# Performance work log

Measured on AMD Instinct MI355X. Metric: run time of the kernel, lower is better.

## Reference

```python
import jax, jax.numpy as jnp
import numpy as np

N = 50000
E = 800000
D_IN, D_HID, D_OUT = 256, 512, 256
LN_EPS = 1e-5


def setup_inputs() -> dict:
    key = jax.random.key(0)
    ks = jax.random.split(key, 8)
    return {
        "v": jax.random.normal(ks[0], (N, D_IN), dtype=jnp.float32),
        "edge_weight": jax.random.uniform(ks[1], (E,), dtype=jnp.float32),
        "epsilon": jnp.zeros((1, 1), dtype=jnp.float32),
        "w1": jax.random.normal(ks[2], (D_HID, D_IN), dtype=jnp.float32) * (1.0 / np.sqrt(D_IN)),
        "b1": jnp.zeros((D_HID,), dtype=jnp.float32),
        "g1": jnp.ones((D_HID,), dtype=jnp.float32),
        "beta1": jnp.zeros((D_HID,), dtype=jnp.float32),
        "w2": jax.random.normal(ks[3], (D_OUT, D_HID), dtype=jnp.float32) * (1.0 / np.sqrt(D_HID)),
        "b2": jnp.zeros((D_OUT,), dtype=jnp.float32),
        "g2": jnp.ones((D_OUT,), dtype=jnp.float32),
        "beta2": jnp.zeros((D_OUT,), dtype=jnp.float32),
        "src": jax.random.randint(ks[4], (E,), 0, N, dtype=jnp.int32),
        "dst": jax.random.randint(ks[5], (E,), 0, N, dtype=jnp.int32),
    }


def _layer_norm(x, g, b):
    mu = jnp.mean(x, axis=-1, keepdims=True)
    var = jnp.mean(jnp.square(x - mu), axis=-1, keepdims=True)
    return (x - mu) * jax.lax.rsqrt(var + LN_EPS) * g + b


def reference(v, edge_weight, epsilon, w1, b1, g1, beta1, w2, b2, g2, beta2, src, dst):
    # sparse adjacency aggregation: agg[dst] += w * v[src]   (torch.sparse.mm(a, v))
    msgs = v[src] * edge_weight[:, None]            # [E, D_IN]
    agg = jax.ops.segment_sum(msgs, dst, num_segments=v.shape[0])  # [N, D_IN]
    h = agg + epsilon * v                            # epsilon residual
    # MLP: Linear -> LayerNorm -> ReLU  (x2)
    h = jax.nn.relu(_layer_norm(h @ w1.T + b1, g1, beta1))
    h = jax.nn.relu(_layer_norm(h @ w2.T + b2, g2, beta2))
    return h
```

## Files before the change

### kernel.cpp

```cpp
#include <hip/hip_runtime.h>

#define D_IN 256
#define D_HID 512
#define D_OUT 256
#define LN_EPS 1e-5f
#define SCAN_B 512

typedef __attribute__((ext_vector_type(8))) short bf16x8;
typedef __attribute__((ext_vector_type(4))) float f32x4;

__device__ __forceinline__ ushort f2bf(float x) {
    union { float f; unsigned u; } c; c.f = x;
    unsigned r = c.u + 0x7FFFu + ((c.u >> 16) & 1u);
    return (ushort)(r >> 16);
}
__device__ __forceinline__ float bf2f(unsigned b) {
    union { unsigned u; float f; } c; c.u = b << 16;
    return c.f;
}

__global__ void prep_kernel(const float* __restrict__ v, const float* __restrict__ w1,
                            const float* __restrict__ w2, ushort* __restrict__ vb,
                            ushort* __restrict__ w1b, ushort* __restrict__ w2b,
                            int* __restrict__ cnt, int n4v, int nzero,
                            int bv, int bw) {
    int b = blockIdx.x, t = threadIdx.x;
    if (b < bv) {
        int i = b * 256 + t;
        if (i < n4v) {
            float4 x = ((const float4*)v)[i];
            ((ushort4*)vb)[i] = make_ushort4(f2bf(x.x), f2bf(x.y), f2bf(x.z), f2bf(x.w));
        }
    } else if (b < bv + bw) {
        int j = (b - bv) * 256 + t;
        if (j < 32768) {
            float4 x = ((const float4*)w1)[j];
            ((ushort4*)w1b)[j] = make_ushort4(f2bf(x.x), f2bf(x.y), f2bf(x.z), f2bf(x.w));
        } else {
            int k = j - 32768;
            float4 x = ((const float4*)w2)[k];
            ((ushort4*)w2b)[k] = make_ushort4(f2bf(x.x), f2bf(x.y), f2bf(x.z), f2bf(x.w));
        }
    } else {
        int i = (b - bv - bw) * 256 + t;
        if (i < nzero) cnt[i] = 0;
    }
}

__global__ void hist_kernel(const int* __restrict__ dst, int* __restrict__ cnt, int E) {
    int e = blockIdx.x * 256 + threadIdx.x;
    if (e < E) atomicAdd(&cnt[dst[e]], 1);
}

__global__ __launch_bounds__(SCAN_B) void scan1_kernel(const int* __restrict__ cnt,
                                                       int* __restrict__ offs,
                                                       int* __restrict__ bsum, int n) {
    __shared__ int s[SCAN_B];
    int i = blockIdx.x * SCAN_B + threadIdx.x;
    int x = (i < n) ? cnt[i] : 0;
    s[threadIdx.x] = x;
    __syncthreads();
    for (int o = 1; o < SCAN_B; o <<= 1) {
        int t = (threadIdx.x >= (unsigned)o) ? s[threadIdx.x - o] : 0;
        __syncthreads();
        s[threadIdx.x] += t;
        __syncthreads();
    }
    if (i < n) offs[i] = s[threadIdx.x] - x;
    if (threadIdx.x == SCAN_B - 1) bsum[blockIdx.x] = s[threadIdx.x];
}

__global__ __launch_bounds__(SCAN_B) void scan3_kernel(int* __restrict__ offs,
                                                       int* __restrict__ cursor,
                                                       const int* __restrict__ bsum,
                                                       int n, int E, int nb) {
    __shared__ int s[SCAN_B];
    int t = threadIdx.x;
    s[t] = (t < nb && t < (int)blockIdx.x) ? bsum[t] : 0;
    __syncthreads();
    for (int o = SCAN_B / 2; o > 0; o >>= 1) {
        if (t < o) s[t] += s[t + o];
        __syncthreads();
    }
    int base = s[0];
    int i = blockIdx.x * SCAN_B + t;
    if (i < n) {
        int v0 = offs[i] + base;
        offs[i] = v0;
        cursor[i] = v0;
    }
    if (i == 0) offs[n] = E;
}

__global__ void fill_kernel(const int* __restrict__ src, const int* __restrict__ dst,
                            const float* __restrict__ ew, int* __restrict__ cursor,
                            int2* __restrict__ perm, int E) {
    int e = blockIdx.x * 256 + threadIdx.x;
    if (e >= E) return;
    int p = atomicAdd(&cursor[dst[e]], 1);
    perm[p] = make_int2(src[e], __float_as_int(ew[e]));
}

__global__ __launch_bounds__(256) void aggregate_kernel(
    const ushort* __restrict__ vb, const float* __restrict__ eps_p,
    const int* __restrict__ offs, const int2* __restrict__ perm,
    ushort* __restrict__ aggb, int N) {
    int node = blockIdx.x * 4 + (threadIdx.x >> 6);
    if (node >= N) return;
    int lane = threadIdx.x & 63;
    int beg = offs[node], end = offs[node + 1];
    float a0 = 0.f, a1 = 0.f, a2 = 0.f, a3 = 0.f;
    float c0 = 0.f, c1 = 0.f, c2 = 0.f, c3 = 0.f;

    int i = beg;
    for (; i + 8 <= end; i += 8) {
        int2 p0 = perm[i + 0], p1 = perm[i + 1], p2 = perm[i + 2], p3 = perm[i + 3];
        int2 p4 = perm[i + 4], p5 = perm[i + 5], p6 = perm[i + 6], p7 = perm[i + 7];
        float w0 = __int_as_float(p0.y), w1 = __int_as_float(p1.y);
        float w2 = __int_as_float(p2.y), w3 = __int_as_float(p3.y);
        float w4 = __int_as_float(p4.y), w5 = __int_as_float(p5.y);
        float w6 = __int_as_float(p6.y), w7 = __int_as_float(p7.y);
        ushort4 r0 = ((const ushort4*)(vb + (size_t)p0.x * D_IN))[lane];
        ushort4 r1 = ((const ushort4*)(vb + (size_t)p1.x * D_IN))[lane];
        ushort4 r2 = ((const ushort4*)(vb + (size_t)p2.x * D_IN))[lane];
        ushort4 r3 = ((const ushort4*)(vb + (size_t)p3.x * D_IN))[lane];
        ushort4 r4 = ((const ushort4*)(vb + (size_t)p4.x * D_IN))[lane];
        ushort4 r5 = ((const ushort4*)(vb + (size_t)p5.x * D_IN))[lane];
        ushort4 r6 = ((const ushort4*)(vb + (size_t)p6.x * D_IN))[lane];
        ushort4 r7 = ((const ushort4*)(vb + (size_t)p7.x * D_IN))[lane];
        a0 += w0 * bf2f(r0.x) + w1 * bf2f(r1.x) + w2 * bf2f(r2.x) + w3 * bf2f(r3.x);
        a1 += w0 * bf2f(r0.y) + w1 * bf2f(r1.y) + w2 * bf2f(r2.y) + w3 * bf2f(r3.y);
        a2 += w0 * bf2f(r0.z) + w1 * bf2f(r1.z) + w2 * bf2f(r2.z) + w3 * bf2f(r3.z);
        a3 += w0 * bf2f(r0.w) + w1 * bf2f(r1.w) + w2 * bf2f(r2.w) + w3 * bf2f(r3.w);
        c0 += w4 * bf2f(r4.x) + w5 * bf2f(r5.x) + w6 * bf2f(r6.x) + w7 * bf2f(r7.x);
        c1 += w4 * bf2f(r4.y) + w5 * bf2f(r5.y) + w6 * bf2f(r6.y) + w7 * bf2f(r7.y);
        c2 += w4 * bf2f(r4.z) + w5 * bf2f(r5.z) + w6 * bf2f(r6.z) + w7 * bf2f(r7.z);
        c3 += w4 * bf2f(r4.w) + w5 * bf2f(r5.w) + w6 * bf2f(r6.w) + w7 * bf2f(r7.w);
    }
    for (; i + 4 <= end; i += 4) {
        int2 p0 = perm[i + 0], p1 = perm[i + 1], p2 = perm[i + 2], p3 = perm[i + 3];
        float w0 = __int_as_float(p0.y), w1 = __int_as_float(p1.y);
        float w2 = __int_as_float(p2.y), w3 = __int_as_float(p3.y);
        ushort4 r0 = ((const ushort4*)(vb + (size_t)p0.x * D_IN))[lane];
        ushort4 r1 = ((const ushort4*)(vb + (size_t)p1.x * D_IN))[lane];
        ushort4 r2 = ((const ushort4*)(vb + (size_t)p2.x * D_IN))[lane];
        ushort4 r3 = ((const ushort4*)(vb + (size_t)p3.x * D_IN))[lane];
        a0 += w0 * bf2f(r0.x) + w1 * bf2f(r1.x) + w2 * bf2f(r2.x) + w3 * bf2f(r3.x);
        a1 += w0 * bf2f(r0.y) + w1 * bf2f(r1.y) + w2 * bf2f(r2.y) + w3 * bf2f(r3.y);
        a2 += w0 * bf2f(r0.z) + w1 * bf2f(r1.z) + w2 * bf2f(r2.z) + w3 * bf2f(r3.z);
        a3 += w0 * bf2f(r0.w) + w1 * bf2f(r1.w) + w2 * bf2f(r2.w) + w3 * bf2f(r3.w);
    }
    for (; i < end; ++i) {
        int2 p = perm[i];
        float w = __int_as_float(p.y);
        ushort4 r = ((const ushort4*)(vb + (size_t)p.x * D_IN))[lane];
        a0 += w * bf2f(r.x); a1 += w * bf2f(r.y);
        a2 += w * bf2f(r.z); a3 += w * bf2f(r.w);
    }
    a0 += c0; a1 += c1; a2 += c2; a3 += c3;
    float eps = eps_p[0];
    ushort4 m = ((const ushort4*)(vb + (size_t)node * D_IN))[lane];
    a0 += eps * bf2f(m.x); a1 += eps * bf2f(m.y);
    a2 += eps * bf2f(m.z); a3 += eps * bf2f(m.w);
    ((ushort4*)(aggb + (size_t)node * D_IN))[lane] =
        make_ushort4(f2bf(a0), f2bf(a1), f2bf(a2), f2bf(a3));
}

#define HS_IDX(row, col) ((row) * 512 + ((col) ^ (((row) & 7) << 3)))

__global__ __launch_bounds__(256, 2) void mlp_kernel(
    const ushort* __restrict__ A, const ushort* __restrict__ w1b,
    const ushort* __restrict__ w2b,
    const float* __restrict__ b1, const float* __restrict__ g1, const float* __restrict__ be1,
    const float* __restrict__ b2, const float* __restrict__ g2, const float* __restrict__ be2,
    float* __restrict__ out, int N) {
    __shared__ ushort hs[32768];
    __shared__ float redf[640];

    int t = threadIdx.x;
    int w = t >> 6, lane = t & 63;
    int row0 = blockIdx.x * 64;
    int fr = lane & 15, q = lane >> 4, kb = q * 8;

    int arow[4];
    #pragma unroll
    for (int m = 0; m < 4; ++m) {
        int ar = row0 + m * 16 + fr;
        if (ar > N - 1) ar = N - 1;
        arow[m] = ar;
    }

    f32x4 acc[4][8];
    #pragma unroll
    for (int m = 0; m < 4; ++m)
        #pragma unroll
        for (int c = 0; c < 8; ++c) {
            f32x4 z = {0.f, 0.f, 0.f, 0.f};
            acc[m][c] = z;
        }

    for (int k0 = 0; k0 < D_IN; k0 += 32) {
        bf16x8 af[4], bf[8];
        #pragma unroll
        for (int m = 0; m < 4; ++m)
            af[m] = *(const bf16x8*)(A + (size_t)arow[m] * D_IN + k0 + kb);
        #pragma unroll
        for (int c = 0; c < 8; ++c)
            bf[c] = *(const bf16x8*)(w1b + (size_t)(w * 128 + c * 16 + fr) * D_IN + k0 + kb);
        #pragma unroll
        for (int m = 0; m < 4; ++m)
            #pragma unroll
            for (int c = 0; c < 8; ++c)
                acc[m][c] = __builtin_amdgcn_mfma_f32_16x16x32_bf16(af[m], bf[c], acc[m][c], 0, 0, 0);
    }

    {
        float bi[8], gg[8], bb[8];
        #pragma unroll
        for (int c = 0; c < 8; ++c) {
            int col = w * 128 + c * 16 + fr;
            bi[c] = b1[col]; gg[c] = g1[col]; bb[c] = be1[col];
        }
        #pragma unroll
        for (int m = 0; m < 4; ++m) {
            #pragma unroll
            for (int r = 0; r < 4; ++r) {
                float s = 0.f, sq = 0.f;
                #pragma unroll
                for (int c = 0; c < 8; ++c) {
                    float x = acc[m][c][r] + bi[c];
                    acc[m][c][r] = x;
                    s += x; sq += x * x;
                }
                #pragma unroll
                for (int o = 1; o < 16; o <<= 1) {
                    s  += __shfl_xor(s, o, 64);
                    sq += __shfl_xor(sq, o, 64);
                }
                if (fr == 0) {
                    int row = m * 16 + q * 4 + r;
                    redf[row * 4 + w]       = s;
                    redf[256 + row * 4 + w] = sq;
                }
            }
        }
        __syncthreads();
        if (t < 64) {
            float s  = redf[t * 4 + 0] + redf[t * 4 + 1] + redf[t * 4 + 2] + redf[t * 4 + 3];
            float sq = redf[256 + t * 4 + 0] + redf[256 + t * 4 + 1] +
                       redf[256 + t * 4 + 2] + redf[256 + t * 4 + 3];
            float mu = s / (float)D_HID;
            float var = sq / (float)D_HID - mu * mu;
            redf[512 + t] = mu;
            redf[576 + t] = rsqrtf(var + LN_EPS);
        }
        __syncthreads();
        #pragma unroll
        for (int m = 0; m < 4; ++m) {
            #pragma unroll
            for (int r = 0; r < 4; ++r) {
                int row = m * 16 + q * 4 + r;
                float mu = redf[512 + row], rs = redf[576 + row];
                #pragma unroll
                for (int c = 0; c < 8; ++c) {
                    int col = w * 128 + c * 16 + fr;
                    float y = (acc[m][c][r] - mu) * rs * gg[c] + bb[c];
                    hs[HS_IDX(row, col)] = f2bf(fmaxf(y, 0.f));
                }
            }
        }
    }
    __syncthreads();

    f32x4 acc2[4][4];
    #pragma unroll
    for (int m = 0; m < 4; ++m)
        #pragma unroll
        for (int c = 0; c < 4; ++c) {
            f32x4 z = {0.f, 0.f, 0.f, 0.f};
            acc2[m][c] = z;
        }

    for (int k0 = 0; k0 < D_HID; k0 += 32) {
        bf16x8 af2[4], bf2[4];
        #pragma unroll
        for (int m = 0; m < 4; ++m)
            af2[m] = *(const bf16x8*)&hs[HS_IDX(m * 16 + fr, k0 + kb)];
        #pragma unroll
        for (int c = 0; c < 4; ++c)
            bf2[c] = *(const bf16x8*)(w2b + (size_t)(w * 64 + c * 16 + fr) * D_HID + k0 + kb);
        #pragma unroll
        for (int m = 0; m < 4; ++m)
            #pragma unroll
            for (int c = 0; c < 4; ++c)
                acc2[m][c] = __builtin_amdgcn_mfma_f32_16x16x32_bf16(af2[m], bf2[c], acc2[m][c], 0, 0, 0);
    }

    {
        float bi[4], gg[4], bb[4];
        #pragma unroll
        for (int c = 0; c < 4; ++c) {
            int col = w * 64 + c * 16 + fr;
            bi[c] = b2[col]; gg[c] = g2[col]; bb[c] = be2[col];
        }
        #pragma unroll
        for (int m = 0; m < 4; ++m) {
            #pragma unroll
            for (int r = 0; r < 4; ++r) {
                float s = 0.f, sq = 0.f;
                #pragma unroll
                for (int c = 0; c < 4; ++c) {
                    float x = acc2[m][c][r] + bi[c];
                    acc2[m][c][r] = x;
                    s += x; sq += x * x;
                }
                #pragma unroll
                for (int o = 1; o < 16; o <<= 1) {
                    s  += __shfl_xor(s, o, 64);
                    sq += __shfl_xor(sq, o, 64);
                }
                if (fr == 0) {
                    int row = m * 16 + q * 4 + r;
                    redf[row * 4 + w]       = s;
                    redf[256 + row * 4 + w] = sq;
                }
            }
        }
        __syncthreads();
        if (t < 64) {
            float s  = redf[t * 4 + 0] + redf[t * 4 + 1] + redf[t * 4 + 2] + redf[t * 4 + 3];
            float sq = redf[256 + t * 4 + 0] + redf[256 + t * 4 + 1] +
                       redf[256 + t * 4 + 2] + redf[256 + t * 4 + 3];
            float mu = s / (float)D_OUT;
            float var = sq / (float)D_OUT - mu * mu;
            redf[512 + t] = mu;
            redf[576 + t] = rsqrtf(var + LN_EPS);
        }
        __syncthreads();
        #pragma unroll
        for (int m = 0; m < 4; ++m) {
            #pragma unroll
            for (int r = 0; r < 4; ++r) {
                int row = m * 16 + q * 4 + r;
                int grow = row0 + row;
                if (grow >= N) continue;
                float mu = redf[512 + row], rs = redf[576 + row];
                #pragma unroll
                for (int c = 0; c < 4; ++c) {
                    int col = w * 64 + c * 16 + fr;
                    float y = (acc2[m][c][r] - mu) * rs * gg[c] + bb[c];
                    out[(size_t)grow * D_OUT + col] = fmaxf(y, 0.f);
                }
            }
        }
    }
}

extern "C" void kernel_launch(void* const* d_in, const int* in_sizes, int n_in,
                              void* d_out, int out_size, void* d_ws, size_t ws_size,
                              hipStream_t stream) {
    const float* v     = (const float*)d_in[0];
    const float* ew    = (const float*)d_in[1];
    const float* eps   = (const float*)d_in[2];
    const float* w1    = (const float*)d_in[3];
    const float* b1    = (const float*)d_in[4];
    const float* g1    = (const float*)d_in[5];
    const float* beta1 = (const float*)d_in[6];
    const float* w2    = (const float*)d_in[7];
    const float* b2    = (const float*)d_in[8];
    const float* g2    = (const float*)d_in[9];
    const float* beta2 = (const float*)d_in[10];
    const int*   src   = (const int*)d_in[11];
    const int*   dst   = (const int*)d_in[12];

    int N = in_sizes[0] / D_IN;
    int E = in_sizes[1];

    float* out = (float*)d_out;

    char* ws = (char*)d_ws;
    size_t off = 0;
    ushort* vb   = (ushort*)(ws + off); off += (size_t)N * D_IN * 2;
    ushort* aggb = (ushort*)(ws + off); off += (size_t)N * D_IN * 2;
    ushort* w1b  = (ushort*)(ws + off); off += (size_t)D_HID * D_IN * 2;
    ushort* w2b  = (ushort*)(ws + off); off += (size_t)D_OUT * D_HID * 2;
    int* offs     = (int*)(ws + off); off += (size_t)(N + 256) * 4;
    int* cursor   = (int*)(ws + off); off += (size_t)(N + 256) * 4;
    int* bsum     = (int*)(ws + off); off += 1024;
    int2* perm    = (int2*)(ws + off); off += (size_t)E * 8;

    int nb = (N + SCAN_B - 1) / SCAN_B;
    int n4v = N * (D_IN / 4);
    int bv = (n4v + 255) / 256;
    int bw = 256;
    int bz = (N + 255) / 256;

    prep_kernel<<<bv + bw + bz, 256, 0, stream>>>(v, w1, w2, vb, w1b, w2b,
                                                  cursor, n4v, N, bv, bw);

    hist_kernel<<<(E + 255) / 256, 256, 0, stream>>>(dst, cursor, E);
    scan1_kernel<<<nb, SCAN_B, 0, stream>>>(cursor, offs, bsum, N);
    scan3_kernel<<<nb, SCAN_B, 0, stream>>>(offs, cursor, bsum, N, E, nb);
    fill_kernel<<<(E + 255) / 256, 256, 0, stream>>>(src, dst, ew, cursor, perm, E);

    aggregate_kernel<<<(N + 3) / 4, 256, 0, stream>>>(vb, eps, offs, perm, aggb, N);

    int mblocks = (N + 63) / 64;
    mlp_kernel<<<mblocks, 256, 0, stream>>>(aggb, w1b, w2b,
                                            b1, g1, beta1, b2, g2, beta2, out, N);
}
```

Before: 360.9 us.

## Stage MLP input tile via direct-to-LDS loads and prepack weights for coalesced double-buffered loads

The weight conversion kernel now writes W1 and W2 in a fragment-packed layout, so each lane's bf16x8 MFMA operand sits in a contiguous, coalesced 16-byte chunk. The mlp kernel loads the 64x256 input tile straight into LDS with global_load_lds using a swizzled layout, instead of each wave re-reading A rows from global memory. Weight fragments are double-buffered in registers so the next k-step's loads overlap the current MFMAs. The cost is higher register pressure from the buffered fragments, which could spill or reduce occupancy, plus an extra barrier.

```diff
diff --git a/kernel.cpp b/kernel.cpp
--- a/kernel.cpp
+++ b/kernel.cpp
@@ -21,7 +21,7 @@
 
 __global__ void prep_kernel(const float* __restrict__ v, const float* __restrict__ w1,
                             const float* __restrict__ w2, ushort* __restrict__ vb,
-                            ushort* __restrict__ w1b, ushort* __restrict__ w2b,
+                            ushort* __restrict__ w1p, ushort* __restrict__ w2p,
                             int* __restrict__ cnt, int n4v, int nzero,
                             int bv, int bw) {
     int b = blockIdx.x, t = threadIdx.x;
@@ -34,12 +34,24 @@
     } else if (b < bv + bw) {
         int j = (b - bv) * 256 + t;
         if (j < 32768) {
+            int f = j * 4;
+            int row = f >> 8, col = f & 255;
             float4 x = ((const float4*)w1)[j];
-            ((ushort4*)w1b)[j] = make_ushort4(f2bf(x.x), f2bf(x.y), f2bf(x.z), f2bf(x.w));
+            int rb = row >> 4, fr = row & 15;
+            int kb32 = col >> 5, q = (col & 31) >> 3, e = col & 7;
+            int chunk = (kb32 * 32 + rb) * 64 + q * 16 + fr;
+            *(ushort4*)(w1p + chunk * 8 + e) =
+                make_ushort4(f2bf(x.x), f2bf(x.y), f2bf(x.z), f2bf(x.w));
         } else {
             int k = j - 32768;
+            int f = k * 4;
+            int row = f >> 9, col = f & 511;
             float4 x = ((const float4*)w2)[k];
-            ((ushort4*)w2b)[k] = make_ushort4(f2bf(x.x), f2bf(x.y), f2bf(x.z), f2bf(x.w));
+            int rb = row >> 4, fr = row & 15;
+            int kb32 = col >> 5, q = (col & 31) >> 3, e = col & 7;
+            int chunk = (kb32 * 16 + rb) * 64 + q * 16 + fr;
+            *(ushort4*)(w2p + chunk * 8 + e) =
+                make_ushort4(f2bf(x.x), f2bf(x.y), f2bf(x.z), f2bf(x.w));
         }
     } else {
         int i = (b - bv - bw) * 256 + t;
@@ -167,10 +179,11 @@
 }
 
 #define HS_IDX(row, col) ((row) * 512 + ((col) ^ (((row) & 7) << 3)))
+#define AT_IDX(row, col) ((row) * 256 + ((col) ^ (((row) & 7) << 3)))
 
 __global__ __launch_bounds__(256, 2) void mlp_kernel(
-    const ushort* __restrict__ A, const ushort* __restrict__ w1b,
-    const ushort* __restrict__ w2b,
+    const ushort* __restrict__ A, const ushort* __restrict__ w1p,
+    const ushort* __restrict__ w2p,
     const float* __restrict__ b1, const float* __restrict__ g1, const float* __restrict__ be1,
     const float* __restrict__ b2, const float* __restrict__ g2, const float* __restrict__ be2,
     float* __restrict__ out, int N) {
@@ -182,13 +195,25 @@
     int row0 = blockIdx.x * 64;
     int fr = lane & 15, q = lane >> 4, kb = q * 8;
 
-    int arow[4];
-    #pragma unroll
-    for (int m = 0; m < 4; ++m) {
-        int ar = row0 + m * 16 + fr;
-        if (ar > N - 1) ar = N - 1;
-        arow[m] = ar;
-    }
+    #pragma unroll
+    for (int j = 0; j < 8; ++j) {
+        int p = (w * 8 + j) * 64 + lane;
+        int row = p >> 5, cbs = p & 31;
+        int colblk = cbs ^ (row & 7);
+        int ar = row0 + row; if (ar > N - 1) ar = N - 1;
+        const ushort* gp = A + (size_t)ar * D_IN + colblk * 8;
+        __builtin_amdgcn_global_load_lds(
+            (const __attribute__((address_space(1))) void*)gp,
+            (__attribute__((address_space(3))) void*)(&hs[(w * 8 + j) * 512]),
+            16, 0, 0);
+    }
+
+    bf16x8 bfb[2][8];
+    #pragma unroll
+    for (int c = 0; c < 8; ++c)
+        bfb[0][c] = *(const bf16x8*)(w1p + (size_t)((0 * 32 + w * 8 + c) * 64 + lane) * 8);
+
+    __syncthreads();
 
     f32x4 acc[4][8];
     #pragma unroll
@@ -199,19 +224,24 @@
             acc[m][c] = z;
         }
 
-    for (int k0 = 0; k0 < D_IN; k0 += 32) {
-        bf16x8 af[4], bf[8];
+    #pragma unroll
+    for (int ks = 0; ks < 8; ++ks) {
+        const int cur = ks & 1, nxt = cur ^ 1;
+        if (ks < 7) {
+            #pragma unroll
+            for (int c = 0; c < 8; ++c)
+                bfb[nxt][c] = *(const bf16x8*)(w1p +
+                    (size_t)(((ks + 1) * 32 + w * 8 + c) * 64 + lane) * 8);
+        }
+        bf16x8 af[4];
         #pragma unroll
         for (int m = 0; m < 4; ++m)
-            af[m] = *(const bf16x8*)(A + (size_t)arow[m] * D_IN + k0 + kb);
-        #pragma unroll
-        for (int c = 0; c < 8; ++c)
-            bf[c] = *(const bf16x8*)(w1b + (size_t)(w * 128 + c * 16 + fr) * D_IN + k0 + kb);
+            af[m] = *(const bf16x8*)&hs[AT_IDX(m * 16 + fr, ks * 32 + kb)];
         #pragma unroll
         for (int m = 0; m < 4; ++m)
             #pragma unroll
             for (int c = 0; c < 8; ++c)
-                acc[m][c] = __builtin_amdgcn_mfma_f32_16x16x32_bf16(af[m], bf[c], acc[m][c], 0, 0, 0);
+                acc[m][c] = __builtin_amdgcn_mfma_f32_16x16x32_bf16(af[m], bfb[cur][c], acc[m][c], 0, 0, 0);
     }
 
     {
@@ -270,6 +300,15 @@
             }
         }
     }
+
+    bf16x8 bf2b[2][4][2];
+    #pragma unroll
+    for (int c = 0; c < 4; ++c)
+        #pragma unroll
+        for (int h = 0; h < 2; ++h)
+            bf2b[0][c][h] = *(const bf16x8*)(w2p +
+                (size_t)(((0 + h) * 16 + w * 4 + c) * 64 + lane) * 8);
+
     __syncthreads();
 
     f32x4 acc2[4][4];
@@ -281,19 +320,30 @@
             acc2[m][c] = z;
         }
 
-    for (int k0 = 0; k0 < D_HID; k0 += 32) {
-        bf16x8 af2[4], bf2[4];
+    #pragma unroll
+    for (int s = 0; s < 8; ++s) {
+        const int cur = s & 1, nxt = cur ^ 1;
+        if (s < 7) {
+            #pragma unroll
+            for (int c = 0; c < 4; ++c)
+                #pragma unroll
+                for (int h = 0; h < 2; ++h)
+                    bf2b[nxt][c][h] = *(const bf16x8*)(w2p +
+                        (size_t)(((2 * (s + 1) + h) * 16 + w * 4 + c) * 64 + lane) * 8);
+        }
+        bf16x8 af2[4][2];
         #pragma unroll
         for (int m = 0; m < 4; ++m)
-            af2[m] = *(const bf16x8*)&hs[HS_IDX(m * 16 + fr, k0 + kb)];
-        #pragma unroll
-        for (int c = 0; c < 4; ++c)
-            bf2[c] = *(const bf16x8*)(w2b + (size_t)(w * 64 + c * 16 + fr) * D_HID + k0 + kb);
+            #pragma unroll
+            for (int h = 0; h < 2; ++h)
+                af2[m][h] = *(const bf16x8*)&hs[HS_IDX(m * 16 + fr, s * 64 + h * 32 + kb)];
         #pragma unroll
         for (int m = 0; m < 4; ++m)
             #pragma unroll
             for (int c = 0; c < 4; ++c)
-                acc2[m][c] = __builtin_amdgcn_mfma_f32_16x16x32_bf16(af2[m], bf2[c], acc2[m][c], 0, 0, 0);
+                #pragma unroll
+                for (int h = 0; h < 2; ++h)
+                    acc2[m][c] = __builtin_amdgcn_mfma_f32_16x16x32_bf16(af2[m][h], bf2b[cur][c][h], acc2[m][c], 0, 0, 0);
     }
 
     {
@@ -382,8 +432,8 @@
     size_t off = 0;
     ushort* vb   = (ushort*)(ws + off); off += (size_t)N * D_IN * 2;
     ushort* aggb = (ushort*)(ws + off); off += (size_t)N * D_IN * 2;
-    ushort* w1b  = (ushort*)(ws + off); off += (size_t)D_HID * D_IN * 2;
-    ushort* w2b  = (ushort*)(ws + off); off += (size_t)D_OUT * D_HID * 2;
+    ushort* w1p  = (ushort*)(ws + off); off += (size_t)D_HID * D_IN * 2;
+    ushort* w2p  = (ushort*)(ws + off); off += (size_t)D_OUT * D_HID * 2;
     int* offs     = (int*)(ws + off); off += (size_t)(N + 256) * 4;
     int* cursor   = (int*)(ws + off); off += (size_t)(N + 256) * 4;
     int* bsum     = (int*)(ws + off); off += 1024;
@@ -395,7 +445,7 @@
     int bw = 256;
     int bz = (N + 255) / 256;
 
-    prep_kernel<<<bv + bw + bz, 256, 0, stream>>>(v, w1, w2, vb, w1b, w2b,
+    prep_kernel<<<bv + bw + bz, 256, 0, stream>>>(v, w1, w2, vb, w1p, w2p,
                                                   cursor, n4v, N, bv, bw);
 
     hist_kernel<<<(E + 255) / 256, 256, 0, stream>>>(dst, cursor, E);
@@ -406,6 +456,6 @@
     aggregate_kernel<<<(N + 3) / 4, 256, 0, stream>>>(vb, eps, offs, perm, aggb, N);
 
     int mblocks = (N + 63) / 64;
-    mlp_kernel<<<mblocks, 256, 0, stream>>>(aggb, w1b, w2b,
+    mlp_kernel<<<mblocks, 256, 0, stream>>>(aggb, w1p, w2p,
                                             b1, g1, beta1, b2, g2, beta2, out, N);
 }
```

Result: faster. 322.6 us (-10.6%).
